# Kernel tuning notes

Hardware: AMD Instinct MI355X
Metric: run time of the kernel (lower is better)

The kernel has to match this reference:

```python
import jax, jax.numpy as jnp
import numpy as np

N, B, F, H = 100000, 128, 512, 256


def setup_inputs() -> dict:
    key = jax.random.key(0)
    ks = jax.random.split(key, 9)
    pos = jax.random.normal(ks[0], (N, 3), dtype=jnp.float32)
    mass_center = jax.random.normal(ks[1], (B, 3), dtype=jnp.float32)
    scaler = jax.random.normal(ks[2], (N, F), dtype=jnp.float32)
    vector = jax.random.normal(ks[3], (N, 3), dtype=jnp.float32)
    batch_index = jax.random.randint(ks[4], (N,), 0, B, dtype=jnp.int64)
    # MLP params (Linear(F,H) -> act -> Linear(H,1)), kaiming-uniform-ish init
    lim1 = 1.0 / np.sqrt(F)
    lim2 = 1.0 / np.sqrt(H)
    W1 = jax.random.uniform(ks[5], (F, H), minval=-lim1, maxval=lim1, dtype=jnp.float32)
    b1 = jax.random.uniform(ks[6], (H,), minval=-lim1, maxval=lim1, dtype=jnp.float32)
    W2 = jax.random.uniform(ks[7], (H, 1), minval=-lim2, maxval=lim2, dtype=jnp.float32)
    b2 = jax.random.uniform(ks[8], (1,), minval=-lim2, maxval=lim2, dtype=jnp.float32)
    return {"pos": pos, "mass_center": mass_center, "scaler": scaler,
            "vector": vector, "batch_index": batch_index,
            "W1": W1, "b1": b1, "W2": W2, "b2": b2}


def reference(pos, mass_center, scaler, vector, batch_index, W1, b1, W2, b2):
    # gather per-graph mass center to nodes: [N,3]
    mass_center_vec = pos - mass_center[batch_index]
    # tiny 2-layer MLP on node scalars: [N,F] -> [N,H] -> [N,1]
    h = jax.nn.silu(scaler @ W1 + b1)
    q_i = h @ W2 + b2                         # [N,1]
    # squared L2 norm of displacement: [N,1]
    r2_i = jnp.sum(mass_center_vec * mass_center_vec, axis=1, keepdims=True)
    # scatter-sum per graph: [B,1]
    out = jax.ops.segment_sum(q_i * r2_i, batch_index, num_segments=B)
    return out
```

## Files before the change

kernel.cpp:

```cpp
#include <hip/hip_runtime.h>
#include <hip/hip_bf16.h>
#include <stdint.h>

#define F_DIM 512
#define H_DIM 256
#define B_DIM 128
#define M_BLK 64
#define NCHUNK 16
#define NBUF 2

typedef __bf16 bf16x8 __attribute__((ext_vector_type(8)));
typedef float  f32x4  __attribute__((ext_vector_type(4)));

__global__ __launch_bounds__(256) void convert_w1_kernel(
    const float* __restrict__ W1, __bf16* __restrict__ W1t) {
    int t = blockIdx.x * 256 + threadIdx.x;
    int c = t >> 9;
    int k = t & 511;
    W1t[t] = (__bf16)W1[k * H_DIM + c];
}

__device__ inline void gload_lds16(const float* g, float* lds) {
    __builtin_amdgcn_global_load_lds(
        (const __attribute__((address_space(1))) uint32_t*)g,
        (__attribute__((address_space(3))) uint32_t*)lds, 16, 0, 0);
}
__device__ inline void gload_lds16b(const __bf16* g, __bf16* lds) {
    __builtin_amdgcn_global_load_lds(
        (const __attribute__((address_space(1))) uint32_t*)g,
        (__attribute__((address_space(3))) uint32_t*)lds, 16, 0, 0);
}

__device__ inline int bswz(int col) { return (col & 3) ^ ((col >> 2) & 3); }

template<bool USE_PARTIAL>
__global__ __launch_bounds__(512, 6) void fused_mlp_kernel(
    const float* __restrict__ pos,
    const float* __restrict__ mass_center,
    const float* __restrict__ scaler,
    const int*   __restrict__ batch_index,
    const __bf16* __restrict__ W1t,
    const float* __restrict__ b1,
    const float* __restrict__ W2,
    const float* __restrict__ b2,
    float* __restrict__ outp,
    int N)
{
    __shared__ float  A_lds[NBUF][M_BLK][32];
    __shared__ __bf16 Bc_lds[NBUF][H_DIM][32];
    __shared__ float  q_lds[M_BLK];
    __shared__ float  pb[B_DIM];

    const int tid    = threadIdx.x;
    const int lane   = tid & 63;
    const int wid    = tid >> 6;
    const int wave_m = wid >> 2;
    const int wave_n = wid & 3;
    const int lrow   = lane & 15;
    const int kq     = (lane >> 4) * 8;
    const int row_base = blockIdx.x * M_BLK;

    if (tid < M_BLK) q_lds[tid] = 0.f;
    if (USE_PARTIAL && tid < B_DIM) pb[tid] = 0.f;

    const int srow = tid >> 3;
    const int sseg = (tid & 7) ^ (srow & 7);
    int grA = row_base + srow; if (grA >= N) grA = N - 1;
    const float* gsA = scaler + (size_t)grA * F_DIM + sseg * 4;

    const int c0 = tid >> 2,         g0 = (tid & 3) ^ bswz(c0);
    const int c1 = (512 + tid) >> 2, g1 = ((512 + tid) & 3) ^ bswz(c1);
    const __bf16* gsB0 = W1t + (size_t)c0 * F_DIM + g0 * 8;
    const __bf16* gsB1 = W1t + (size_t)c1 * F_DIM + g1 * 8;

#define STAGE(buf, c) do {                                                      \
        gload_lds16 (gsA  + (c) * 32, &A_lds[(buf)][0][0] + wid * 256);         \
        gload_lds16b(gsB0 + (c) * 32, &Bc_lds[(buf)][0][0] + wid * 512);        \
        gload_lds16b(gsB1 + (c) * 32, &Bc_lds[(buf)][0][0] + 4096 + wid * 512); \
    } while (0)

    f32x4 acc[2][4];
    #pragma unroll
    for (int mi = 0; mi < 2; ++mi)
        #pragma unroll
        for (int ni = 0; ni < 4; ++ni)
            acc[mi][ni] = (f32x4){0.f, 0.f, 0.f, 0.f};

    STAGE(0, 0);
    STAGE(1, 1);

    #pragma unroll
    for (int kc = 0; kc < NCHUNK; ++kc) {
        if (kc < NCHUNK - 1) asm volatile("s_waitcnt vmcnt(3)" ::: "memory");
        else                 asm volatile("s_waitcnt vmcnt(0)" ::: "memory");
        __builtin_amdgcn_s_barrier();

        const int buf = kc & 1;
        bf16x8 af[2];
        #pragma unroll
        for (int mi = 0; mi < 2; ++mi) {
            const int rA = wave_m * 32 + mi * 16 + lrow;
            const int sw = (rA & 7) << 4;
            const char* rb = (const char*)&A_lds[buf][0][0] + rA * 128;
            f32x4 a0 = *(const f32x4*)(rb + ((kq * 4) ^ sw));
            f32x4 a1 = *(const f32x4*)(rb + ((kq * 4 + 16) ^ sw));
            #pragma unroll
            for (int j = 0; j < 4; ++j) {
                af[mi][j]     = (__bf16)a0[j];
                af[mi][4 + j] = (__bf16)a1[j];
            }
        }
        bf16x8 bfrag[4];
        #pragma unroll
        for (int ni = 0; ni < 4; ++ni) {
            const int col = wave_n * 64 + ni * 16 + lrow;
            const int ps  = (lane >> 4) ^ bswz(col);
            bfrag[ni] = *(const bf16x8*)((const char*)&Bc_lds[buf][0][0]
                                         + col * 64 + ps * 16);
        }
        #pragma unroll
        for (int mi = 0; mi < 2; ++mi)
            #pragma unroll
            for (int ni = 0; ni < 4; ++ni)
                acc[mi][ni] = __builtin_amdgcn_mfma_f32_16x16x32_bf16(
                    af[mi], bfrag[ni], acc[mi][ni], 0, 0, 0);

        __builtin_amdgcn_s_barrier();
        if (kc + 2 < NCHUNK)
            STAGE(buf, kc + 2);
    }
#undef STAGE

    float qp[2][4];
    #pragma unroll
    for (int mi = 0; mi < 2; ++mi)
        #pragma unroll
        for (int r = 0; r < 4; ++r) qp[mi][r] = 0.f;

    #pragma unroll
    for (int ni = 0; ni < 4; ++ni) {
        int c = wave_n * 64 + ni * 16 + lrow;
        float b1c = b1[c];
        float w2c = W2[c];
        #pragma unroll
        for (int mi = 0; mi < 2; ++mi)
            #pragma unroll
            for (int r = 0; r < 4; ++r) {
                float h = acc[mi][ni][r] + b1c;
                float s = h / (1.0f + __expf(-h));
                qp[mi][r] += s * w2c;
            }
    }
    #pragma unroll
    for (int off = 1; off < 16; off <<= 1)
        #pragma unroll
        for (int mi = 0; mi < 2; ++mi)
            #pragma unroll
            for (int r = 0; r < 4; ++r)
                qp[mi][r] += __shfl_xor(qp[mi][r], off, 64);

    if ((lane & 15) == 0) {
        int rgrp = lane >> 4;
        #pragma unroll
        for (int mi = 0; mi < 2; ++mi)
            #pragma unroll
            for (int r = 0; r < 4; ++r)
                atomicAdd(&q_lds[wave_m * 32 + mi * 16 + rgrp * 4 + r], qp[mi][r]);
    }
    __syncthreads();

    if (tid < M_BLK) {
        int grow = row_base + tid;
        if (grow < N) {
            float q  = q_lds[tid] + b2[0];
            int   bi = batch_index[grow];
            float dx = pos[grow * 3 + 0] - mass_center[bi * 3 + 0];
            float dy = pos[grow * 3 + 1] - mass_center[bi * 3 + 1];
            float dz = pos[grow * 3 + 2] - mass_center[bi * 3 + 2];
            float val = q * (dx * dx + dy * dy + dz * dz);
            if (USE_PARTIAL) atomicAdd(&pb[bi], val);
            else             atomicAdd(&outp[bi], val);
        }
    }
    if (USE_PARTIAL) {
        __syncthreads();
        if (tid < B_DIM)
            outp[(size_t)blockIdx.x * B_DIM + tid] = pb[tid];
    }
}

__global__ __launch_bounds__(256) void reduce_partials_kernel(
    const float* __restrict__ partial, float* __restrict__ out, int nblk) {
    int b = blockIdx.x;
    float s = 0.f;
    for (int i = threadIdx.x; i < nblk; i += 256)
        s += partial[(size_t)i * B_DIM + b];
    #pragma unroll
    for (int off = 1; off < 64; off <<= 1)
        s += __shfl_xor(s, off, 64);
    __shared__ float wsum[4];
    if ((threadIdx.x & 63) == 0) wsum[threadIdx.x >> 6] = s;
    __syncthreads();
    if (threadIdx.x == 0)
        out[b] = wsum[0] + wsum[1] + wsum[2] + wsum[3];
}

extern "C" void kernel_launch(void* const* d_in, const int* in_sizes, int n_in,
                              void* d_out, int out_size, void* d_ws, size_t ws_size,
                              hipStream_t stream) {
    const float* pos         = (const float*)d_in[0];
    const float* mass_center = (const float*)d_in[1];
    const float* scaler      = (const float*)d_in[2];
    const int*   batch_index = (const int*)d_in[4];
    const float* W1          = (const float*)d_in[5];
    const float* b1          = (const float*)d_in[6];
    const float* W2          = (const float*)d_in[7];
    const float* b2          = (const float*)d_in[8];
    float* out = (float*)d_out;
    (void)n_in; (void)out_size;

    int N = in_sizes[0] / 3;
    int nblk = (N + M_BLK - 1) / M_BLK;

    size_t w1t_bytes  = (size_t)F_DIM * H_DIM * sizeof(__bf16);
    size_t part_bytes = (size_t)nblk * B_DIM * sizeof(float);

    __bf16* W1t = (__bf16*)d_ws;
    convert_w1_kernel<<<(F_DIM * H_DIM) / 256, 256, 0, stream>>>(W1, W1t);

    if (ws_size >= w1t_bytes + part_bytes) {
        float* partial = (float*)((char*)d_ws + w1t_bytes);
        fused_mlp_kernel<true><<<nblk, 512, 0, stream>>>(
            pos, mass_center, scaler, batch_index, W1t, b1, W2, b2, partial, N);
        reduce_partials_kernel<<<B_DIM, 256, 0, stream>>>(partial, out, nblk);
    } else {
        hipMemsetAsync(out, 0, B_DIM * sizeof(float), stream);
        fused_mlp_kernel<false><<<nblk, 512, 0, stream>>>(
            pos, mass_center, scaler, batch_index, W1t, b1, W2, b2, out, N);
    }
}
```

Baseline: 78.10 us.

## Double block rows to 128 with 1024 threads and drop partial-reduce kernel

Each block now processes 128 rows with 1024 threads (16 waves), so each thread stages one W1 chunk instead of two, and every W1 tile is reused across twice as many rows. The per-block partial buffer and the separate reduce kernel are removed; each row atomically adds directly to the global 128-entry output after a memset. This halves the block count and W1 reloads and removes a launch, in exchange for heavy global atomic contention on 128 addresses and larger blocks that may limit occupancy (1024 threads, roughly 48KB of LDS).

New measurement: 182.5 us. 134% more time.

```diff
diff --git a/kernel.cpp b/kernel.cpp
--- a/kernel.cpp
+++ b/kernel.cpp
@@ -5,7 +5,7 @@
 #define F_DIM 512
 #define H_DIM 256
 #define B_DIM 128
-#define M_BLK 64
+#define M_BLK 128
 #define NCHUNK 16
 #define NBUF 2
 
@@ -33,8 +33,7 @@
 
 __device__ inline int bswz(int col) { return (col & 3) ^ ((col >> 2) & 3); }
 
-template<bool USE_PARTIAL>
-__global__ __launch_bounds__(512, 6) void fused_mlp_kernel(
+__global__ __launch_bounds__(1024, 8) void fused_mlp_kernel(
     const float* __restrict__ pos,
     const float* __restrict__ mass_center,
     const float* __restrict__ scaler,
@@ -43,13 +42,12 @@
     const float* __restrict__ b1,
     const float* __restrict__ W2,
     const float* __restrict__ b2,
-    float* __restrict__ outp,
+    float* __restrict__ out,
     int N)
 {
     __shared__ float  A_lds[NBUF][M_BLK][32];
     __shared__ __bf16 Bc_lds[NBUF][H_DIM][32];
     __shared__ float  q_lds[M_BLK];
-    __shared__ float  pb[B_DIM];
 
     const int tid    = threadIdx.x;
     const int lane   = tid & 63;
@@ -61,22 +59,19 @@
     const int row_base = blockIdx.x * M_BLK;
 
     if (tid < M_BLK) q_lds[tid] = 0.f;
-    if (USE_PARTIAL && tid < B_DIM) pb[tid] = 0.f;
 
     const int srow = tid >> 3;
     const int sseg = (tid & 7) ^ (srow & 7);
     int grA = row_base + srow; if (grA >= N) grA = N - 1;
     const float* gsA = scaler + (size_t)grA * F_DIM + sseg * 4;
 
-    const int c0 = tid >> 2,         g0 = (tid & 3) ^ bswz(c0);
-    const int c1 = (512 + tid) >> 2, g1 = ((512 + tid) & 3) ^ bswz(c1);
-    const __bf16* gsB0 = W1t + (size_t)c0 * F_DIM + g0 * 8;
-    const __bf16* gsB1 = W1t + (size_t)c1 * F_DIM + g1 * 8;
-
-#define STAGE(buf, c) do {                                                      \
-        gload_lds16 (gsA  + (c) * 32, &A_lds[(buf)][0][0] + wid * 256);         \
-        gload_lds16b(gsB0 + (c) * 32, &Bc_lds[(buf)][0][0] + wid * 512);        \
-        gload_lds16b(gsB1 + (c) * 32, &Bc_lds[(buf)][0][0] + 4096 + wid * 512); \
+    const int c0 = tid >> 2;
+    const int g0 = (tid & 3) ^ bswz(c0);
+    const __bf16* gsB = W1t + (size_t)c0 * F_DIM + g0 * 8;
+
+#define STAGE(buf, c) do {                                                 \
+        gload_lds16 (gsA + (c) * 32, &A_lds[(buf)][0][0] + wid * 256);     \
+        gload_lds16b(gsB + (c) * 32, &Bc_lds[(buf)][0][0] + wid * 512);    \
     } while (0)
 
     f32x4 acc[2][4];
@@ -91,7 +86,7 @@
 
     #pragma unroll
     for (int kc = 0; kc < NCHUNK; ++kc) {
-        if (kc < NCHUNK - 1) asm volatile("s_waitcnt vmcnt(3)" ::: "memory");
+        if (kc < NCHUNK - 1) asm volatile("s_waitcnt vmcnt(2)" ::: "memory");
         else                 asm volatile("s_waitcnt vmcnt(0)" ::: "memory");
         __builtin_amdgcn_s_barrier();
 
@@ -177,32 +172,9 @@
             float dx = pos[grow * 3 + 0] - mass_center[bi * 3 + 0];
             float dy = pos[grow * 3 + 1] - mass_center[bi * 3 + 1];
             float dz = pos[grow * 3 + 2] - mass_center[bi * 3 + 2];
-            float val = q * (dx * dx + dy * dy + dz * dz);
-            if (USE_PARTIAL) atomicAdd(&pb[bi], val);
-            else             atomicAdd(&outp[bi], val);
+            atomicAdd(&out[bi], q * (dx * dx + dy * dy + dz * dz));
         }
     }
-    if (USE_PARTIAL) {
-        __syncthreads();
-        if (tid < B_DIM)
-            outp[(size_t)blockIdx.x * B_DIM + tid] = pb[tid];
-    }
-}
-
-__global__ __launch_bounds__(256) void reduce_partials_kernel(
-    const float* __restrict__ partial, float* __restrict__ out, int nblk) {
-    int b = blockIdx.x;
-    float s = 0.f;
-    for (int i = threadIdx.x; i < nblk; i += 256)
-        s += partial[(size_t)i * B_DIM + b];
-    #pragma unroll
-    for (int off = 1; off < 64; off <<= 1)
-        s += __shfl_xor(s, off, 64);
-    __shared__ float wsum[4];
-    if ((threadIdx.x & 63) == 0) wsum[threadIdx.x >> 6] = s;
-    __syncthreads();
-    if (threadIdx.x == 0)
-        out[b] = wsum[0] + wsum[1] + wsum[2] + wsum[3];
 }
 
 extern "C" void kernel_launch(void* const* d_in, const int* in_sizes, int n_in,
@@ -217,25 +189,14 @@
     const float* W2          = (const float*)d_in[7];
     const float* b2          = (const float*)d_in[8];
     float* out = (float*)d_out;
-    (void)n_in; (void)out_size;
+    (void)n_in; (void)out_size; (void)ws_size;
 
     int N = in_sizes[0] / 3;
     int nblk = (N + M_BLK - 1) / M_BLK;
 
-    size_t w1t_bytes  = (size_t)F_DIM * H_DIM * sizeof(__bf16);
-    size_t part_bytes = (size_t)nblk * B_DIM * sizeof(float);
-
     __bf16* W1t = (__bf16*)d_ws;
+    hipMemsetAsync(out, 0, B_DIM * sizeof(float), stream);
     convert_w1_kernel<<<(F_DIM * H_DIM) / 256, 256, 0, stream>>>(W1, W1t);
-
-    if (ws_size >= w1t_bytes + part_bytes) {
-        float* partial = (float*)((char*)d_ws + w1t_bytes);
-        fused_mlp_kernel<true><<<nblk, 512, 0, stream>>>(
-            pos, mass_center, scaler, batch_index, W1t, b1, W2, b2, partial, N);
-        reduce_partials_kernel<<<B_DIM, 256, 0, stream>>>(partial, out, nblk);
-    } else {
-        hipMemsetAsync(out, 0, B_DIM * sizeof(float), stream);
-        fused_mlp_kernel<false><<<nblk, 512, 0, stream>>>(
-            pos, mass_center, scaler, batch_index, W1t, b1, W2, b2, out, N);
-    }
-}
+    fused_mlp_kernel<<<nblk, 1024, 0, stream>>>(
+        pos, mass_center, scaler, batch_index, W1t, b1, W2, b2, out, N);
+}
```
